# Optimization experiments

Measured on AMD Instinct MI355X. Metric: run time of the kernel, lower is better.

## Reference

```python
import jax, jax.numpy as jnp
import numpy as np

DIM = 384
HEADS = 6
HEAD_DIM = DIM // HEADS
HIDDEN = int(DIM * 4.0)
LS_INIT = 1e-5
EPS = 1e-5


def _ln(x, w, b):
    mu = jnp.mean(x, axis=-1, keepdims=True)
    var = jnp.var(x, axis=-1, keepdims=True)
    return (x - mu) * jax.lax.rsqrt(var + EPS) * w + b


def setup_inputs() -> dict:
    key = jax.random.key(0)
    ks = jax.random.split(key, 12)
    s = 0.02
    eye = jnp.eye(HIDDEN, dtype=jnp.float32)
    return {
        "x": jax.random.normal(ks[0], (8, 2048, DIM), dtype=jnp.float32),
        "qkv_w": jax.random.normal(ks[1], (3 * DIM, DIM), dtype=jnp.float32) * s,
        "qkv_b": jnp.zeros((3 * DIM,), dtype=jnp.float32),
        "proj_w": jax.random.normal(ks[2], (DIM, DIM), dtype=jnp.float32) * s,
        "proj_b": jnp.zeros((DIM,), dtype=jnp.float32),
        "fc1_w": jax.random.normal(ks[3], (HIDDEN, DIM), dtype=jnp.float32) * s,
        "fc1_b": jnp.zeros((HIDDEN,), dtype=jnp.float32),
        "eye1_w": eye + jax.random.normal(ks[4], (HIDDEN, HIDDEN), dtype=jnp.float32) * s,
        "eye2_w": eye + jax.random.normal(ks[5], (HIDDEN, HIDDEN), dtype=jnp.float32) * s,
        "fc2_w": jax.random.normal(ks[6], (DIM, HIDDEN), dtype=jnp.float32) * s,
        "fc2_b": jnp.zeros((DIM,), dtype=jnp.float32),
        "norm1_w": jnp.ones((DIM,), dtype=jnp.float32),
        "norm1_b": jnp.zeros((DIM,), dtype=jnp.float32),
        "norm2_w": jnp.ones((DIM,), dtype=jnp.float32),
        "norm2_b": jnp.zeros((DIM,), dtype=jnp.float32),
        "ls1_gamma": jnp.full((DIM,), LS_INIT, dtype=jnp.float32),
        "ls2_gamma": jnp.full((DIM,), LS_INIT, dtype=jnp.float32),
    }


def reference(x, qkv_w, qkv_b, proj_w, proj_b, fc1_w, fc1_b, eye1_w, eye2_w,
              fc2_w, fc2_b, norm1_w, norm1_b, norm2_w, norm2_b, ls1_gamma, ls2_gamma):
    B, N, C = x.shape
    scale = HEAD_DIM ** -0.5

    # ---- attention branch ----
    h = _ln(x, norm1_w, norm1_b)
    qkv = h @ qkv_w.T + qkv_b                      # [B,N,3C]
    qkv = qkv.reshape(B, N, 3, HEADS, HEAD_DIM)
    q = qkv[:, :, 0].transpose(0, 2, 1, 3) * scale  # [B,H,N,D]
    k = qkv[:, :, 1].transpose(0, 2, 1, 3)
    v = qkv[:, :, 2].transpose(0, 2, 1, 3)
    attn = jax.nn.softmax(jnp.einsum('bhnd,bhmd->bhnm', q, k), axis=-1)  # [B,H,N,N]
    o = jnp.einsum('bhnm,bhmd->bhnd', attn, v)
    o = o.transpose(0, 2, 1, 3).reshape(B, N, C)
    o = o @ proj_w.T + proj_b
    x = x + o * ls1_gamma

    # ---- extended MLP branch (timm Mlp norm is Identity) ----
    h2 = _ln(x, norm2_w, norm2_b)
    a = jax.nn.gelu(h2 @ fc1_w.T + fc1_b, approximate=False)
    a = (a @ eye1_w.T) @ eye2_w.T
    a = a @ fc2_w.T + fc2_b
    return x + a * ls2_gamma
```

## Files before the change

kernel.cpp:

```cpp
#include <hip/hip_runtime.h>
#include <math.h>

#define DIM 384
#define HEADS 6
#define HEAD_DIM 64
#define HIDDEN 1536
#define BATCH 8
#define SEQ 2048
#define TOKENS (BATCH * SEQ)

typedef __bf16 bf16;
typedef float f32x4 __attribute__((ext_vector_type(4)));
typedef float f32x16 __attribute__((ext_vector_type(16)));
typedef int i32x2 __attribute__((ext_vector_type(2)));
typedef int i32x4 __attribute__((ext_vector_type(4)));
typedef int i32x8 __attribute__((ext_vector_type(8)));

#define GLOAD_LDS(gp, lp)                                                      \
    __builtin_amdgcn_global_load_lds(                                          \
        (const __attribute__((address_space(1))) void*)(gp),                   \
        (__attribute__((address_space(3))) void*)(lp), 16, 0, 0)

__device__ __forceinline__ unsigned char to_fp8(float v) {
    return (unsigned char)(__builtin_amdgcn_cvt_pk_fp8_f32(v, v, 0, false) & 0xff);
}

__device__ __forceinline__ i32x8 pack8(i32x4 lo, i32x4 hi) {
    i32x8 r;
#pragma unroll
    for (int j = 0; j < 4; j++) { r[j] = lo[j]; r[4 + j] = hi[j]; }
    return r;
}

#define NW_QKV  (1152 * 384)
#define NW_PROJ (384 * 384)
#define NW_FC1  (1536 * 384)
#define NW_EYE  (1536 * 1536)
#define NW_FC2  (384 * 1536)
#define NW_ALL3 (NW_QKV + NW_PROJ + NW_FC1 + NW_FC2)

template <int EPI>
__device__ __forceinline__ void gemm_core(const unsigned char* __restrict__ A,
                                          const unsigned char* __restrict__ W,
                                          const float* __restrict__ bias,
                                          float* __restrict__ outf,
                                          const float* __restrict__ resid,
                                          const float* __restrict__ gamma,
                                          unsigned char* __restrict__ vtb8,
                                          unsigned char* __restrict__ out8,
                                          int N, int K, int bx, int by,
                                          unsigned char* As, unsigned char* Bs) {
    int tid = threadIdx.x;
    int wave = tid >> 6, lane = tid & 63;
    int l15 = lane & 15, quad = lane >> 4;
    int bm = by * 128, bn = bx * 128;
    int wm = (wave & 1) * 64, wn = (wave >> 1) * 64;
    f32x4 acc[4][4] = {};

    for (int k0 = 0; k0 < K; k0 += 128) {
#pragma unroll
        for (int i = 0; i < 4; i++) {
            int slot = i * 256 + tid;
            int rr = slot >> 3;
            int gg = (slot & 7) ^ (rr & 7);
            GLOAD_LDS(A + (size_t)(bm + rr) * K + k0 + gg * 16,
                      (char*)As + (i * 256 + wave * 64) * 16);
            GLOAD_LDS(W + (size_t)(bn + rr) * K + k0 + gg * 16,
                      (char*)Bs + (i * 256 + wave * 64) * 16);
        }
        __syncthreads();
        i32x8 af[4], bfr[4];
#pragma unroll
        for (int mt = 0; mt < 4; mt++) {
            int rA = wm + mt * 16 + l15;
            const i32x4* p = (const i32x4*)(As + 128 * rA);
            af[mt] = pack8(p[(2 * quad) ^ (rA & 7)], p[(2 * quad + 1) ^ (rA & 7)]);
        }
#pragma unroll
        for (int nt = 0; nt < 4; nt++) {
            int rB = wn + nt * 16 + l15;
            const i32x4* p = (const i32x4*)(Bs + 128 * rB);
            bfr[nt] = pack8(p[(2 * quad) ^ (rB & 7)], p[(2 * quad + 1) ^ (rB & 7)]);
        }
#pragma unroll
        for (int mt = 0; mt < 4; mt++)
#pragma unroll
            for (int nt = 0; nt < 4; nt++)
                acc[mt][nt] = __builtin_amdgcn_mfma_scale_f32_16x16x128_f8f6f4(
                    af[mt], bfr[nt], acc[mt][nt], 0, 0,
                    0, 0x7f7f7f7f, 0, 0x7f7f7f7f);
        __syncthreads();
    }

#pragma unroll
    for (int mt = 0; mt < 4; mt++) {
#pragma unroll
        for (int nt = 0; nt < 4; nt++) {
            int col = bn + wn + nt * 16 + l15;
            int row0 = bm + wm + mt * 16 + quad * 4;
            float v[4];
#pragma unroll
            for (int r = 0; r < 4; r++) {
                v[r] = acc[mt][nt][r];
                if (EPI >= 2) v[r] += bias[col];
                if (EPI == 2) v[r] = 0.5f * v[r] * (1.f + erff(v[r] * 0.70710678118654752f));
            }
            if (EPI == 3) {
#pragma unroll
                for (int r = 0; r < 4; r++) {
                    size_t idx = (size_t)(row0 + r) * N + col;
                    outf[idx] = resid[idx] + v[r] * gamma[col];
                }
            } else if (EPI == 4) {
                if (col < 768) {
                    float sc = (col < 384) ? 0.180336880f : 1.f;
#pragma unroll
                    for (int r = 0; r < 4; r++)
                        out8[(size_t)(row0 + r) * 768 + col] = to_fp8(v[r] * sc);
                } else {
                    int hd = col - 768;
                    int b = row0 >> 11;
                    int n0 = row0 & 2047;
                    int p = __builtin_amdgcn_cvt_pk_fp8_f32(v[0], v[1], 0, false);
                    p = __builtin_amdgcn_cvt_pk_fp8_f32(v[2], v[3], p, true);
                    *(int*)(vtb8 + ((size_t)(b * 384 + hd) << 11) + n0) = p;
                }
            } else {
#pragma unroll
                for (int r = 0; r < 4; r++)
                    out8[(size_t)(row0 + r) * N + col] = to_fp8(v[r]);
            }
        }
    }
}

template <int EPI>
__global__ __launch_bounds__(256) void gemm_f8(const unsigned char* __restrict__ A,
                                               const unsigned char* __restrict__ W,
                                               const float* __restrict__ bias,
                                               float* __restrict__ outf,
                                               const float* __restrict__ resid,
                                               const float* __restrict__ gamma,
                                               unsigned char* __restrict__ vtb8,
                                               unsigned char* __restrict__ out8,
                                               int N, int K) {
    __shared__ __attribute__((aligned(16))) unsigned char As[128 * 128];
    __shared__ __attribute__((aligned(16))) unsigned char Bs[128 * 128];
    gemm_core<EPI>(A, W, bias, outf, resid, gamma, vtb8, out8, N, K,
                   blockIdx.x, blockIdx.y, As, Bs);
}

__global__ __launch_bounds__(256) void fused_pre(const float* __restrict__ x,
                                                 const float* __restrict__ n1w,
                                                 const float* __restrict__ n1b,
                                                 unsigned char* __restrict__ hbuf8,
                                                 const float* __restrict__ e1,
                                                 unsigned char* __restrict__ e1t8,
                                                 const float* __restrict__ e2,
                                                 unsigned char* __restrict__ e2t8,
                                                 const float* __restrict__ qkv,
                                                 const float* __restrict__ proj,
                                                 const float* __restrict__ fc1,
                                                 const float* __restrict__ fc2,
                                                 unsigned char* __restrict__ w8) {
    __shared__ float tb[64][65];
    int bid = blockIdx.x;
    int tid = threadIdx.x;
    if (bid < 4096) {
        int wave = tid >> 6, lane = tid & 63;
        int tok = bid * 4 + wave;
        const float* xr = x + (size_t)tok * DIM;
        float v[6];
        float s = 0.f;
#pragma unroll
        for (int i = 0; i < 6; i++) { v[i] = xr[lane + 64 * i]; s += v[i]; }
#pragma unroll
        for (int m = 1; m < 64; m <<= 1) s += __shfl_xor(s, m, 64);
        float mu = s * (1.f / DIM);
        float q = 0.f;
#pragma unroll
        for (int i = 0; i < 6; i++) { float d = v[i] - mu; q += d * d; }
#pragma unroll
        for (int m = 1; m < 64; m <<= 1) q += __shfl_xor(q, m, 64);
        float rstd = rsqrtf(q * (1.f / DIM) + 1e-5f);
        unsigned char* orow = hbuf8 + (size_t)tok * DIM;
#pragma unroll
        for (int i = 0; i < 6; i++) {
            int c = lane + 64 * i;
            orow[c] = to_fp8((v[i] - mu) * rstd * n1w[c] + n1b[c]);
        }
    } else if (bid < 5248) {
        int g = bid - 4096;
        const float* src = e1;
        unsigned char* dst = e1t8;
        if (g >= 576) { g -= 576; src = e2; dst = e2t8; }
        int r0 = (g / 24) * 64, c0 = (g % 24) * 64;
        int tc = tid & 63, tr = tid >> 6;
#pragma unroll
        for (int i = 0; i < 16; i++) {
            int r = tr + 4 * i;
            tb[r][tc] = src[(size_t)(r0 + r) * 1536 + c0 + tc];
        }
        __syncthreads();
        int on = tid >> 2;
        int ok0 = (tid & 3) * 16;
        i32x4 pk;
#pragma unroll
        for (int q = 0; q < 4; q++) {
            int p = __builtin_amdgcn_cvt_pk_fp8_f32(tb[ok0 + 4 * q + 0][on],
                                                    tb[ok0 + 4 * q + 1][on], 0, false);
            p = __builtin_amdgcn_cvt_pk_fp8_f32(tb[ok0 + 4 * q + 2][on],
                                                tb[ok0 + 4 * q + 3][on], p, true);
            pk[q] = p;
        }
        *(i32x4*)(dst + (size_t)(c0 + on) * 1536 + r0 + ok0) = pk;
    } else {
        int q4 = (bid - 5248) * 256 + tid;
        int i = q4 * 4;
        int j = i;
        const float* src;
        if (j < NW_QKV) src = qkv;
        else if ((j -= NW_QKV) < NW_PROJ) src = proj;
        else if ((j -= NW_PROJ) < NW_FC1) src = fc1;
        else { j -= NW_FC1; src = fc2; }
        float4 v = *(const float4*)(src + j);
        int p = __builtin_amdgcn_cvt_pk_fp8_f32(v.x, v.y, 0, false);
        p = __builtin_amdgcn_cvt_pk_fp8_f32(v.z, v.w, p, true);
        *(int*)(w8 + i) = p;
    }
}

__global__ __launch_bounds__(256) void gemm_qkv_prep(const unsigned char* __restrict__ hbuf8,
                                                     const unsigned char* __restrict__ wqkv8,
                                                     const float* __restrict__ qkv_b,
                                                     unsigned char* __restrict__ vtb8,
                                                     unsigned char* __restrict__ qk8,
                                                     const unsigned char* __restrict__ wfc28,
                                                     const unsigned char* __restrict__ e2t8,
                                                     unsigned char* __restrict__ wfe8) {
    __shared__ __attribute__((aligned(16))) unsigned char As[128 * 128];
    __shared__ __attribute__((aligned(16))) unsigned char Bs[128 * 128];
    int bid = blockIdx.x;
    if (bid < 36) {
        gemm_core<0>(wfc28, e2t8, nullptr, nullptr, nullptr, nullptr, nullptr, wfe8,
                     1536, 1536, bid % 12, bid / 12, As, Bs);
    } else {
        int g = bid - 36;
        gemm_core<4>(hbuf8, wqkv8, qkv_b, nullptr, nullptr, nullptr, vtb8, qk8,
                     1152, 384, g % 9, g / 9, As, Bs);
    }
}

__device__ __forceinline__ void projln_core(const unsigned char* __restrict__ A,
                                            const unsigned char* __restrict__ W,
                                            const float* __restrict__ bias,
                                            const float* __restrict__ resid,
                                            const float* __restrict__ gamma,
                                            const float* __restrict__ n2w,
                                            const float* __restrict__ n2b,
                                            float* __restrict__ x1,
                                            unsigned char* __restrict__ hbuf8,
                                            int bidx, unsigned char* As, unsigned char* Bs) {
    int tid = threadIdx.x;
    int wave = tid >> 6, lane = tid & 63;
    int l15 = lane & 15, quad = lane >> 4;
    int bm = bidx * 64;
    int wm = wave * 16;
    f32x4 acc[24];
#pragma unroll
    for (int i = 0; i < 24; i++) acc[i] = (f32x4){0.f, 0.f, 0.f, 0.f};

    const int K = 384;
    for (int k0 = 0; k0 < K; k0 += 128) {
#pragma unroll
        for (int i = 0; i < 2; i++) {
            int slot = i * 256 + tid;
            int rr = slot >> 3, gg = (slot & 7) ^ (rr & 7);
            GLOAD_LDS(A + (size_t)(bm + rr) * K + k0 + gg * 16, (char*)As + slot * 16);
        }
#pragma unroll
        for (int i = 0; i < 12; i++) {
            int slot = i * 256 + tid;
            int rr = slot >> 3, gg = (slot & 7) ^ (rr & 7);
            GLOAD_LDS(W + (size_t)rr * K + k0 + gg * 16, (char*)Bs + slot * 16);
        }
        __syncthreads();
        int rA = wm + l15;
        const i32x4* pa = (const i32x4*)(As + 128 * rA);
        i32x8 af = pack8(pa[(2 * quad) ^ (rA & 7)], pa[(2 * quad + 1) ^ (rA & 7)]);
#pragma unroll
        for (int nt = 0; nt < 24; nt++) {
            int rB = nt * 16 + l15;
            const i32x4* pb = (const i32x4*)(Bs + 128 * rB);
            i32x8 bf = pack8(pb[(2 * quad) ^ (rB & 7)], pb[(2 * quad + 1) ^ (rB & 7)]);
            acc[nt] = __builtin_amdgcn_mfma_scale_f32_16x16x128_f8f6f4(
                af, bf, acc[nt], 0, 0, 0, 0x7f7f7f7f, 0, 0x7f7f7f7f);
        }
        __syncthreads();
    }

    int row0 = bm + wm + quad * 4;
#pragma unroll
    for (int nt = 0; nt < 24; nt++) {
        int col = nt * 16 + l15;
        float bi = bias[col], ga = gamma[col];
#pragma unroll
        for (int r = 0; r < 4; r++) {
            size_t idx = (size_t)(row0 + r) * DIM + col;
            float v = resid[idx] + (acc[nt][r] + bi) * ga;
            x1[idx] = v;
            acc[nt][r] = v;
        }
    }
#pragma unroll
    for (int r = 0; r < 4; r++) {
        float s = 0.f;
#pragma unroll
        for (int nt = 0; nt < 24; nt++) s += acc[nt][r];
#pragma unroll
        for (int m = 1; m < 16; m <<= 1) s += __shfl_xor(s, m, 64);
        float mu = s * (1.f / DIM);
        float q = 0.f;
#pragma unroll
        for (int nt = 0; nt < 24; nt++) { float d = acc[nt][r] - mu; q += d * d; }
#pragma unroll
        for (int m = 1; m < 16; m <<= 1) q += __shfl_xor(q, m, 64);
        float rstd = rsqrtf(q * (1.f / DIM) + 1e-5f);
        unsigned char* orow = hbuf8 + (size_t)(row0 + r) * DIM;
#pragma unroll
        for (int nt = 0; nt < 24; nt++) {
            int col = nt * 16 + l15;
            orow[col] = to_fp8((acc[nt][r] - mu) * rstd * n2w[col] + n2b[col]);
        }
    }
}

__global__ __launch_bounds__(256) void gemm_projln_prep(const unsigned char* __restrict__ obuf8,
                                                        const unsigned char* __restrict__ wproj8,
                                                        const float* __restrict__ proj_b,
                                                        const float* __restrict__ x,
                                                        const float* __restrict__ ls1,
                                                        const float* __restrict__ n2w,
                                                        const float* __restrict__ n2b,
                                                        float* __restrict__ x1,
                                                        unsigned char* __restrict__ hbuf8,
                                                        const unsigned char* __restrict__ wfe8,
                                                        const unsigned char* __restrict__ e1t8,
                                                        unsigned char* __restrict__ wc8) {
    __shared__ __attribute__((aligned(16))) unsigned char smem[448 * 128];
    int bid = blockIdx.x;
    if (bid < 36) {
        gemm_core<0>(wfe8, e1t8, nullptr, nullptr, nullptr, nullptr, nullptr, wc8,
                     1536, 1536, bid % 12, bid / 12, smem, smem + 128 * 128);
    } else {
        projln_core(obuf8, wproj8, proj_b, x, ls1, n2w, n2b, x1, hbuf8,
                    bid - 36, smem, smem + 64 * 128);
    }
}

__global__ __launch_bounds__(256, 3) void attn_kernel(const unsigned char* __restrict__ qk8,
                                                      const unsigned char* __restrict__ vtb8,
                                                      unsigned char* __restrict__ o) {
    __shared__ __attribute__((aligned(16))) unsigned char Ks[2][128 * 64];
    __shared__ __attribute__((aligned(16))) unsigned char Vts[2][64 * 128];
    int tid = threadIdx.x, wave = tid >> 6, lane = tid & 63;
    int l31 = lane & 31, h = lane >> 5;
    int bh = blockIdx.y;
    int b = bh / HEADS, hh = bh - b * HEADS;
    int qr0 = blockIdx.x * 128 + wave * 32;
    const unsigned char* base = qk8 + (size_t)b * SEQ * 768;
    const unsigned char* vbase = vtb8 + ((size_t)bh << 17);

    int kr0 = tid >> 2, kr1 = (tid + 256) >> 2, ks = tid & 3;
    const unsigned char* kg0 = base + (size_t)kr0 * 768 + 384 + hh * 64 + 16 * (ks ^ ((kr0 >> 1) & 3));
    const unsigned char* kg1 = base + (size_t)kr1 * 768 + 384 + hh * 64 + 16 * (ks ^ ((kr1 >> 1) & 3));
    int vr0 = tid >> 3, vr1 = (tid + 256) >> 3, vs = tid & 7;
    const unsigned char* vg0 = vbase + ((size_t)vr0 << 11) + 16 * (vs ^ ((vr0 >> 1) & 3));
    const unsigned char* vg1 = vbase + ((size_t)vr1 << 11) + 16 * (vs ^ ((vr1 >> 1) & 3));
    int lo0 = tid * 16, lo1 = (tid + 256) * 16;

    i32x8 aq = *(const i32x8*)(base + (size_t)(qr0 + l31) * 768 + hh * 64 + 32 * h);

    f32x16 oa0 = {}, oa1 = {};
    float lsum = 0.f;
    int swr = (l31 >> 1) & 3;

    GLOAD_LDS(kg0, (char*)Ks[0] + lo0);
    GLOAD_LDS(kg1, (char*)Ks[0] + lo1);
    GLOAD_LDS(vg0, (char*)Vts[0] + lo0);
    GLOAD_LDS(vg1, (char*)Vts[0] + lo1);
    __syncthreads();

    for (int kt = 0; kt < SEQ / 128; kt++) {
        const unsigned char* Kc = Ks[kt & 1];
        const unsigned char* Vc = Vts[kt & 1];
        if (kt + 1 < SEQ / 128) {
            char* kn = (char*)Ks[(kt + 1) & 1];
            char* vn = (char*)Vts[(kt + 1) & 1];
            size_t kadv = (size_t)(kt + 1) * 128 * 768;
            int vadv = (kt + 1) * 128;
            GLOAD_LDS(kg0 + kadv, kn + lo0);
            GLOAD_LDS(kg1 + kadv, kn + lo1);
            GLOAD_LDS(vg0 + vadv, vn + lo0);
            GLOAD_LDS(vg1 + vadv, vn + lo1);
        }

        int pk[4][4];
#pragma unroll
        for (int mi = 0; mi < 4; mi++) {
            int rK = 32 * mi + l31;
            const i32x4* kp = (const i32x4*)(Kc + rK * 64);
            i32x8 ak = pack8(kp[(2 * h + 0) ^ swr], kp[(2 * h + 1) ^ swr]);
            f32x16 s = {};
            s = __builtin_amdgcn_mfma_scale_f32_32x32x64_f8f6f4(
                ak, aq, s, 0, 0, 0, 0x7f7f7f7f, 0, 0x7f7f7f7f);
#pragma unroll
            for (int g = 0; g < 4; g++) {
                float p0 = __builtin_amdgcn_exp2f(s[4 * g + 0]);
                float p1 = __builtin_amdgcn_exp2f(s[4 * g + 1]);
                float p2 = __builtin_amdgcn_exp2f(s[4 * g + 2]);
                float p3 = __builtin_amdgcn_exp2f(s[4 * g + 3]);
                lsum += (p0 + p1) + (p2 + p3);
                int pkv = __builtin_amdgcn_cvt_pk_fp8_f32(p0, p1, 0, false);
                pkv = __builtin_amdgcn_cvt_pk_fp8_f32(p2, p3, pkv, true);
                pk[mi][g] = pkv;
            }
        }

        i32x8 ap0, ap1;
#pragma unroll
        for (int g = 0; g < 4; g++) {
            i32x2 r0 = __builtin_amdgcn_permlane32_swap(pk[0][g], pk[1][g], false, false);
            ap0[2 * g] = r0[0];
            ap0[2 * g + 1] = r0[1];
            i32x2 r1 = __builtin_amdgcn_permlane32_swap(pk[2][g], pk[3][g], false, false);
            ap1[2 * g] = r1[0];
            ap1[2 * g + 1] = r1[1];
        }

        {
            const i32x4* vp0 = (const i32x4*)(Vc + l31 * 128);
            const i32x4* vp1 = (const i32x4*)(Vc + (32 + l31) * 128);
            i32x8 bv00 = pack8(vp0[(2 * h + 0) ^ swr], vp0[(2 * h + 1) ^ swr]);
            i32x8 bv01 = pack8(vp0[4 + ((2 * h + 0) ^ swr)], vp0[4 + ((2 * h + 1) ^ swr)]);
            i32x8 bv10 = pack8(vp1[(2 * h + 0) ^ swr], vp1[(2 * h + 1) ^ swr]);
            i32x8 bv11 = pack8(vp1[4 + ((2 * h + 0) ^ swr)], vp1[4 + ((2 * h + 1) ^ swr)]);
            oa0 = __builtin_amdgcn_mfma_scale_f32_32x32x64_f8f6f4(
                ap0, bv00, oa0, 0, 0, 0, 0x7f7f7f7f, 0, 0x7f7f7f7f);
            oa0 = __builtin_amdgcn_mfma_scale_f32_32x32x64_f8f6f4(
                ap1, bv01, oa0, 0, 0, 0, 0x7f7f7f7f, 0, 0x7f7f7f7f);
            oa1 = __builtin_amdgcn_mfma_scale_f32_32x32x64_f8f6f4(
                ap0, bv10, oa1, 0, 0, 0, 0x7f7f7f7f, 0, 0x7f7f7f7f);
            oa1 = __builtin_amdgcn_mfma_scale_f32_32x32x64_f8f6f4(
                ap1, bv11, oa1, 0, 0, 0, 0x7f7f7f7f, 0, 0x7f7f7f7f);
        }
        __syncthreads();
    }

    lsum += __shfl_xor(lsum, 32, 64);

#pragma unroll
    for (int g = 0; g < 4; g++) {
#pragma unroll
        for (int r4 = 0; r4 < 4; r4++) {
            int qloc = r4 + 8 * g + 4 * h;
            float inv = 1.f / __shfl(lsum, qloc, 64);
            int r = 4 * g + r4;
            unsigned char* orow = o + ((size_t)(b * SEQ + qr0 + qloc)) * DIM + hh * 64;
            orow[l31]      = to_fp8(oa0[r] * inv);
            orow[32 + l31] = to_fp8(oa1[r] * inv);
        }
    }
}

extern "C" void kernel_launch(void* const* d_in, const int* in_sizes, int n_in,
                              void* d_out, int out_size, void* d_ws, size_t ws_size,
                              hipStream_t stream) {
    const float* x      = (const float*)d_in[0];
    const float* qkv_w  = (const float*)d_in[1];
    const float* qkv_b  = (const float*)d_in[2];
    const float* proj_w = (const float*)d_in[3];
    const float* proj_b = (const float*)d_in[4];
    const float* fc1_w  = (const float*)d_in[5];
    const float* fc1_b  = (const float*)d_in[6];
    const float* eye1_w = (const float*)d_in[7];
    const float* eye2_w = (const float*)d_in[8];
    const float* fc2_w  = (const float*)d_in[9];
    const float* fc2_b  = (const float*)d_in[10];
    const float* n1w    = (const float*)d_in[11];
    const float* n1b    = (const float*)d_in[12];
    const float* n2w    = (const float*)d_in[13];
    const float* n2b    = (const float*)d_in[14];
    const float* ls1    = (const float*)d_in[15];
    const float* ls2    = (const float*)d_in[16];
    float* out = (float*)d_out;

    char* w = (char*)d_ws;
    size_t off = 0;
    unsigned char* w8 = (unsigned char*)(w + off); off += (size_t)NW_ALL3;
    unsigned char* wqkv8  = w8;
    unsigned char* wproj8 = wqkv8 + NW_QKV;
    unsigned char* wfc18  = wproj8 + NW_PROJ;
    unsigned char* wfc28  = wfc18 + NW_FC1;
    unsigned char* e1t8  = (unsigned char*)(w + off); off += (size_t)NW_EYE;
    unsigned char* e2t8  = (unsigned char*)(w + off); off += (size_t)NW_EYE;
    unsigned char* wfe8  = (unsigned char*)(w + off); off += (size_t)NW_FC2;
    unsigned char* wc8   = (unsigned char*)(w + off); off += (size_t)NW_FC2;
    unsigned char* hbuf8 = (unsigned char*)(w + off); off += (size_t)TOKENS * DIM;
    unsigned char* qk8   = (unsigned char*)(w + off); off += (size_t)TOKENS * 768;
    unsigned char* vtb8  = (unsigned char*)(w + off); off += (size_t)TOKENS * DIM;
    unsigned char* obuf8 = (unsigned char*)(w + off); off += (size_t)TOKENS * DIM;
    unsigned char* abuf8 = (unsigned char*)(w + off); off += (size_t)TOKENS * HIDDEN;
    float* x1   = (float*)(w + off); off += (size_t)TOKENS * DIM * 4;

    fused_pre<<<4096 + 1152 + 1728, 256, 0, stream>>>(
        x, n1w, n1b, hbuf8, eye1_w, e1t8, eye2_w, e2t8,
        qkv_w, proj_w, fc1_w, fc2_w, w8);

    gemm_qkv_prep<<<36 + 1152, 256, 0, stream>>>(hbuf8, wqkv8, qkv_b, vtb8, qk8,
                                                 wfc28, e2t8, wfe8);

    attn_kernel<<<dim3(SEQ / 128, BATCH * HEADS), 256, 0, stream>>>(qk8, vtb8, obuf8);

    gemm_projln_prep<<<36 + 256, 256, 0, stream>>>(obuf8, wproj8, proj_b, x, ls1,
                                                   n2w, n2b, x1, hbuf8,
                                                   wfe8, e1t8, wc8);

    gemm_f8<2><<<dim3(1536 / 128, TOKENS / 128), 256, 0, stream>>>(
        hbuf8, wfc18, fc1_b, nullptr, nullptr, nullptr, nullptr, abuf8, 1536, 384);

    gemm_f8<3><<<dim3(384 / 128, TOKENS / 128), 256, 0, stream>>>(
        abuf8, wc8, fc2_b, out, x1, ls2, nullptr, nullptr, 384, 1536);
}
```

Before: 276.5 us.

## Move eye1 weight-folding GEMM from proj-LN kernel into attention launch

The side GEMM that folds eye1 into the fc2 weights (wfe8 x e1t8 -> wc8) moves from the proj+LayerNorm kernel into the attention launch as 36 extra blocks, and proj+LN becomes a standalone kernel. The aim is to hide this GEMM behind the long attention phase and to give the proj+LN kernel its own smaller shared-memory footprint. In exchange, attention loses its launch bound of 3 blocks per SM and shares a 32 KB shared buffer, which may change occupancy, and the extra GEMM blocks could delay attention's tail.

```diff
diff --git a/kernel.cpp b/kernel.cpp
--- a/kernel.cpp
+++ b/kernel.cpp
@@ -251,20 +251,21 @@
     }
 }
 
-__device__ __forceinline__ void projln_core(const unsigned char* __restrict__ A,
-                                            const unsigned char* __restrict__ W,
-                                            const float* __restrict__ bias,
-                                            const float* __restrict__ resid,
-                                            const float* __restrict__ gamma,
-                                            const float* __restrict__ n2w,
-                                            const float* __restrict__ n2b,
-                                            float* __restrict__ x1,
-                                            unsigned char* __restrict__ hbuf8,
-                                            int bidx, unsigned char* As, unsigned char* Bs) {
+__global__ __launch_bounds__(256) void gemm_projln(const unsigned char* __restrict__ A,
+                                                   const unsigned char* __restrict__ W,
+                                                   const float* __restrict__ bias,
+                                                   const float* __restrict__ resid,
+                                                   const float* __restrict__ gamma,
+                                                   const float* __restrict__ n2w,
+                                                   const float* __restrict__ n2b,
+                                                   float* __restrict__ x1,
+                                                   unsigned char* __restrict__ hbuf8) {
+    __shared__ __attribute__((aligned(16))) unsigned char As[64 * 128];
+    __shared__ __attribute__((aligned(16))) unsigned char Bs[384 * 128];
     int tid = threadIdx.x;
     int wave = tid >> 6, lane = tid & 63;
     int l15 = lane & 15, quad = lane >> 4;
-    int bm = bidx * 64;
+    int bm = blockIdx.x * 64;
     int wm = wave * 16;
     f32x4 acc[24];
 #pragma unroll
@@ -335,39 +336,16 @@
     }
 }
 
-__global__ __launch_bounds__(256) void gemm_projln_prep(const unsigned char* __restrict__ obuf8,
-                                                        const unsigned char* __restrict__ wproj8,
-                                                        const float* __restrict__ proj_b,
-                                                        const float* __restrict__ x,
-                                                        const float* __restrict__ ls1,
-                                                        const float* __restrict__ n2w,
-                                                        const float* __restrict__ n2b,
-                                                        float* __restrict__ x1,
-                                                        unsigned char* __restrict__ hbuf8,
-                                                        const unsigned char* __restrict__ wfe8,
-                                                        const unsigned char* __restrict__ e1t8,
-                                                        unsigned char* __restrict__ wc8) {
-    __shared__ __attribute__((aligned(16))) unsigned char smem[448 * 128];
-    int bid = blockIdx.x;
-    if (bid < 36) {
-        gemm_core<0>(wfe8, e1t8, nullptr, nullptr, nullptr, nullptr, nullptr, wc8,
-                     1536, 1536, bid % 12, bid / 12, smem, smem + 128 * 128);
-    } else {
-        projln_core(obuf8, wproj8, proj_b, x, ls1, n2w, n2b, x1, hbuf8,
-                    bid - 36, smem, smem + 64 * 128);
-    }
-}
-
-__global__ __launch_bounds__(256, 3) void attn_kernel(const unsigned char* __restrict__ qk8,
-                                                      const unsigned char* __restrict__ vtb8,
-                                                      unsigned char* __restrict__ o) {
-    __shared__ __attribute__((aligned(16))) unsigned char Ks[2][128 * 64];
-    __shared__ __attribute__((aligned(16))) unsigned char Vts[2][64 * 128];
+__device__ __forceinline__ void attn_core(const unsigned char* __restrict__ qk8,
+                                          const unsigned char* __restrict__ vtb8,
+                                          unsigned char* __restrict__ o,
+                                          int bx, int bh, unsigned char* smem) {
+    unsigned char* Ks0 = smem;
+    unsigned char* Vts0 = smem + 2 * 128 * 64;
     int tid = threadIdx.x, wave = tid >> 6, lane = tid & 63;
     int l31 = lane & 31, h = lane >> 5;
-    int bh = blockIdx.y;
     int b = bh / HEADS, hh = bh - b * HEADS;
-    int qr0 = blockIdx.x * 128 + wave * 32;
+    int qr0 = bx * 128 + wave * 32;
     const unsigned char* base = qk8 + (size_t)b * SEQ * 768;
     const unsigned char* vbase = vtb8 + ((size_t)bh << 17);
 
@@ -385,18 +363,18 @@
     float lsum = 0.f;
     int swr = (l31 >> 1) & 3;
 
-    GLOAD_LDS(kg0, (char*)Ks[0] + lo0);
-    GLOAD_LDS(kg1, (char*)Ks[0] + lo1);
-    GLOAD_LDS(vg0, (char*)Vts[0] + lo0);
-    GLOAD_LDS(vg1, (char*)Vts[0] + lo1);
+    GLOAD_LDS(kg0, (char*)Ks0 + lo0);
+    GLOAD_LDS(kg1, (char*)Ks0 + lo1);
+    GLOAD_LDS(vg0, (char*)Vts0 + lo0);
+    GLOAD_LDS(vg1, (char*)Vts0 + lo1);
     __syncthreads();
 
     for (int kt = 0; kt < SEQ / 128; kt++) {
-        const unsigned char* Kc = Ks[kt & 1];
-        const unsigned char* Vc = Vts[kt & 1];
+        const unsigned char* Kc = Ks0 + (kt & 1) * 128 * 64;
+        const unsigned char* Vc = Vts0 + (kt & 1) * 64 * 128;
         if (kt + 1 < SEQ / 128) {
-            char* kn = (char*)Ks[(kt + 1) & 1];
-            char* vn = (char*)Vts[(kt + 1) & 1];
+            char* kn = (char*)Ks0 + ((kt + 1) & 1) * 128 * 64;
+            char* vn = (char*)Vts0 + ((kt + 1) & 1) * 64 * 128;
             size_t kadv = (size_t)(kt + 1) * 128 * 768;
             int vadv = (kt + 1) * 128;
             GLOAD_LDS(kg0 + kadv, kn + lo0);
@@ -470,6 +448,23 @@
             orow[l31]      = to_fp8(oa0[r] * inv);
             orow[32 + l31] = to_fp8(oa1[r] * inv);
         }
+    }
+}
+
+__global__ __launch_bounds__(256) void attn_prep(const unsigned char* __restrict__ qk8,
+                                                 const unsigned char* __restrict__ vtb8,
+                                                 unsigned char* __restrict__ o,
+                                                 const unsigned char* __restrict__ wfe8,
+                                                 const unsigned char* __restrict__ e1t8,
+                                                 unsigned char* __restrict__ wc8) {
+    __shared__ __attribute__((aligned(16))) unsigned char smem[32768];
+    int bid = blockIdx.x;
+    if (bid < 36) {
+        gemm_core<0>(wfe8, e1t8, nullptr, nullptr, nullptr, nullptr, nullptr, wc8,
+                     1536, 1536, bid % 12, bid / 12, smem, smem + 128 * 128);
+    } else {
+        int g = bid - 36;
+        attn_core(qk8, vtb8, o, g & 15, g >> 4, smem);
     }
 }
 
@@ -520,11 +515,10 @@
     gemm_qkv_prep<<<36 + 1152, 256, 0, stream>>>(hbuf8, wqkv8, qkv_b, vtb8, qk8,
                                                  wfc28, e2t8, wfe8);
 
-    attn_kernel<<<dim3(SEQ / 128, BATCH * HEADS), 256, 0, stream>>>(qk8, vtb8, obuf8);
-
-    gemm_projln_prep<<<36 + 256, 256, 0, stream>>>(obuf8, wproj8, proj_b, x, ls1,
-                                                   n2w, n2b, x1, hbuf8,
-                                                   wfe8, e1t8, wc8);
+    attn_prep<<<36 + 768, 256, 0, stream>>>(qk8, vtb8, obuf8, wfe8, e1t8, wc8);
+
+    gemm_projln<<<TOKENS / 64, 256, 0, stream>>>(obuf8, wproj8, proj_b, x, ls1,
+                                                 n2w, n2b, x1, hbuf8);
 
     gemm_f8<2><<<dim3(1536 / 128, TOKENS / 128), 256, 0, stream>>>(
         hbuf8, wfc18, fc1_b, nullptr, nullptr, nullptr, nullptr, abuf8, 1536, 384);
```

Result: no change. 273.2 us (-1.2%).

## Move eye1 weight-fold GEMM into qkv kernel with atomic flag dependency

Applied to the files above, without the earlier changes.

The second weight-folding GEMM (fc2·eye2 result times eye1) now runs inside the qkv GEMM launch. Its blocks spin on a global counter that the first fold's blocks increment after finishing. The projection+LayerNorm kernel becomes a standalone launch without the 36 large GEMM blocks, which removes load imbalance on that kernel's critical path. The cost is extra work in the qkv launch and a spin-wait that relies on producer blocks being scheduled before consumers.

```diff
diff --git a/kernel.cpp b/kernel.cpp
--- a/kernel.cpp
+++ b/kernel.cpp
@@ -162,10 +162,12 @@
                                                  const float* __restrict__ proj,
                                                  const float* __restrict__ fc1,
                                                  const float* __restrict__ fc2,
-                                                 unsigned char* __restrict__ w8) {
+                                                 unsigned char* __restrict__ w8,
+                                                 int* __restrict__ flag) {
     __shared__ float tb[64][65];
     int bid = blockIdx.x;
     int tid = threadIdx.x;
+    if (bid == 0 && tid == 0) *flag = 0;
     if (bid < 4096) {
         int wave = tid >> 6, lane = tid & 63;
         int tok = bid * 4 + wave;
@@ -237,34 +239,53 @@
                                                      unsigned char* __restrict__ qk8,
                                                      const unsigned char* __restrict__ wfc28,
                                                      const unsigned char* __restrict__ e2t8,
-                                                     unsigned char* __restrict__ wfe8) {
+                                                     unsigned char* wfe8,
+                                                     const unsigned char* __restrict__ e1t8,
+                                                     unsigned char* wc8,
+                                                     int* flag) {
     __shared__ __attribute__((aligned(16))) unsigned char As[128 * 128];
     __shared__ __attribute__((aligned(16))) unsigned char Bs[128 * 128];
     int bid = blockIdx.x;
+    int tid = threadIdx.x;
     if (bid < 36) {
         gemm_core<0>(wfc28, e2t8, nullptr, nullptr, nullptr, nullptr, nullptr, wfe8,
                      1536, 1536, bid % 12, bid / 12, As, Bs);
-    } else {
+        __threadfence();
+        __syncthreads();
+        if (tid == 0)
+            __hip_atomic_fetch_add(flag, 1, __ATOMIC_RELEASE, __HIP_MEMORY_SCOPE_AGENT);
+    } else if (bid < 36 + 1152) {
         int g = bid - 36;
         gemm_core<4>(hbuf8, wqkv8, qkv_b, nullptr, nullptr, nullptr, vtb8, qk8,
                      1152, 384, g % 9, g / 9, As, Bs);
-    }
-}
-
-__device__ __forceinline__ void projln_core(const unsigned char* __restrict__ A,
-                                            const unsigned char* __restrict__ W,
-                                            const float* __restrict__ bias,
-                                            const float* __restrict__ resid,
-                                            const float* __restrict__ gamma,
-                                            const float* __restrict__ n2w,
-                                            const float* __restrict__ n2b,
-                                            float* __restrict__ x1,
-                                            unsigned char* __restrict__ hbuf8,
-                                            int bidx, unsigned char* As, unsigned char* Bs) {
+    } else {
+        if (tid == 0) {
+            while (__hip_atomic_load(flag, __ATOMIC_ACQUIRE, __HIP_MEMORY_SCOPE_AGENT) < 36)
+                __builtin_amdgcn_s_sleep(8);
+        }
+        __syncthreads();
+        __threadfence();
+        int g = bid - (36 + 1152);
+        gemm_core<0>(wfe8, e1t8, nullptr, nullptr, nullptr, nullptr, nullptr, wc8,
+                     1536, 1536, g % 12, g / 12, As, Bs);
+    }
+}
+
+__global__ __launch_bounds__(256) void gemm_projln(const unsigned char* __restrict__ A,
+                                                   const unsigned char* __restrict__ W,
+                                                   const float* __restrict__ bias,
+                                                   const float* __restrict__ resid,
+                                                   const float* __restrict__ gamma,
+                                                   const float* __restrict__ n2w,
+                                                   const float* __restrict__ n2b,
+                                                   float* __restrict__ x1,
+                                                   unsigned char* __restrict__ hbuf8) {
+    __shared__ __attribute__((aligned(16))) unsigned char As[64 * 128];
+    __shared__ __attribute__((aligned(16))) unsigned char Bs[384 * 128];
     int tid = threadIdx.x;
     int wave = tid >> 6, lane = tid & 63;
     int l15 = lane & 15, quad = lane >> 4;
-    int bm = bidx * 64;
+    int bm = blockIdx.x * 64;
     int wm = wave * 16;
     f32x4 acc[24];
 #pragma unroll
@@ -332,29 +353,6 @@
             int col = nt * 16 + l15;
             orow[col] = to_fp8((acc[nt][r] - mu) * rstd * n2w[col] + n2b[col]);
         }
-    }
-}
-
-__global__ __launch_bounds__(256) void gemm_projln_prep(const unsigned char* __restrict__ obuf8,
-                                                        const unsigned char* __restrict__ wproj8,
-                                                        const float* __restrict__ proj_b,
-                                                        const float* __restrict__ x,
-                                                        const float* __restrict__ ls1,
-                                                        const float* __restrict__ n2w,
-                                                        const float* __restrict__ n2b,
-                                                        float* __restrict__ x1,
-                                                        unsigned char* __restrict__ hbuf8,
-                                                        const unsigned char* __restrict__ wfe8,
-                                                        const unsigned char* __restrict__ e1t8,
-                                                        unsigned char* __restrict__ wc8) {
-    __shared__ __attribute__((aligned(16))) unsigned char smem[448 * 128];
-    int bid = blockIdx.x;
-    if (bid < 36) {
-        gemm_core<0>(wfe8, e1t8, nullptr, nullptr, nullptr, nullptr, nullptr, wc8,
-                     1536, 1536, bid % 12, bid / 12, smem, smem + 128 * 128);
-    } else {
-        projln_core(obuf8, wproj8, proj_b, x, ls1, n2w, n2b, x1, hbuf8,
-                    bid - 36, smem, smem + 64 * 128);
     }
 }
 
@@ -512,19 +510,19 @@
     unsigned char* obuf8 = (unsigned char*)(w + off); off += (size_t)TOKENS * DIM;
     unsigned char* abuf8 = (unsigned char*)(w + off); off += (size_t)TOKENS * HIDDEN;
     float* x1   = (float*)(w + off); off += (size_t)TOKENS * DIM * 4;
+    int* flag   = (int*)(w + off); off += 256;
 
     fused_pre<<<4096 + 1152 + 1728, 256, 0, stream>>>(
         x, n1w, n1b, hbuf8, eye1_w, e1t8, eye2_w, e2t8,
-        qkv_w, proj_w, fc1_w, fc2_w, w8);
-
-    gemm_qkv_prep<<<36 + 1152, 256, 0, stream>>>(hbuf8, wqkv8, qkv_b, vtb8, qk8,
-                                                 wfc28, e2t8, wfe8);
+        qkv_w, proj_w, fc1_w, fc2_w, w8, flag);
+
+    gemm_qkv_prep<<<36 + 1152 + 36, 256, 0, stream>>>(hbuf8, wqkv8, qkv_b, vtb8, qk8,
+                                                      wfc28, e2t8, wfe8, e1t8, wc8, flag);
 
     attn_kernel<<<dim3(SEQ / 128, BATCH * HEADS), 256, 0, stream>>>(qk8, vtb8, obuf8);
 
-    gemm_projln_prep<<<36 + 256, 256, 0, stream>>>(obuf8, wproj8, proj_b, x, ls1,
-                                                   n2w, n2b, x1, hbuf8,
-                                                   wfe8, e1t8, wc8);
+    gemm_projln<<<TOKENS / 64, 256, 0, stream>>>(obuf8, wproj8, proj_b, x, ls1,
+                                                 n2w, n2b, x1, hbuf8);
 
     gemm_f8<2><<<dim3(1536 / 128, TOKENS / 128), 256, 0, stream>>>(
         hbuf8, wfc18, fc1_b, nullptr, nullptr, nullptr, nullptr, abuf8, 1536, 384);
```

Result: slower. 291.5 us (+5.4%).
